# Performance work log

Measured on AMD Instinct MI355X. Metric: run time of the kernel, lower is better.

Reference implementation:

```python
import jax, jax.numpy as jnp
import numpy as np

VOCAB, EMBED, HIDDEN = 32000, 512, 1024
B, T = 2, 2048
LN_EPS = 1e-5


def setup_inputs() -> dict:
    key = jax.random.key(0)
    ks = jax.random.split(key, 12)

    def xavier(k, fan_in, fan_out):
        lim = float(np.sqrt(6.0 / (fan_in + fan_out)))
        return jax.random.uniform(k, (fan_in, fan_out), jnp.float32, -lim, lim)

    return {
        "tokens": jax.random.randint(ks[0], (B, T), 0, VOCAB),
        "E": xavier(ks[1], VOCAB, EMBED),                    # embedding table
        "Wc": xavier(ks[2], EMBED, HIDDEN),                  # fc_current (stored [in,out])
        "bc": jnp.full((HIDDEN,), 0.01, jnp.float32),
        "Wh": xavier(ks[3], EMBED, HIDDEN),                  # fc_context
        "bh": jnp.full((HIDDEN,), 0.01, jnp.float32),
        "Wm": xavier(ks[4], 2 * HIDDEN, HIDDEN),             # fc_merge
        "bm": jnp.full((HIDDEN,), 0.01, jnp.float32),
        "Wo": xavier(ks[5], HIDDEN, VOCAB),                  # fc_out
        "bo": jnp.full((VOCAB,), 0.01, jnp.float32),
        "ln_w": jnp.ones((HIDDEN,), jnp.float32),
        "ln_b": jnp.zeros((HIDDEN,), jnp.float32),
    }


def reference(tokens, E, Wc, bc, Wh, bh, Wm, bm, Wo, bo, ln_w, ln_b):
    emb = E[tokens]  # [B, T, D]
    # history mean at step t = mean(emb[:, :t]); at t==0 the module uses current embed
    csum = jnp.cumsum(emb, axis=1)
    counts = jnp.arange(1, T, dtype=emb.dtype)[None, :, None]
    hist_mean = jnp.concatenate([emb[:, :1], csum[:, :-1] / counts], axis=1)  # [B,T,D]

    cur_enc = jax.nn.relu(jnp.einsum("btd,dh->bth", emb, Wc) + bc)
    hist_enc = jax.nn.relu(jnp.einsum("btd,dh->bth", hist_mean, Wh) + bh)
    merged = jnp.concatenate([cur_enc, hist_enc], axis=-1)  # [B,T,2H]
    merged = jax.nn.relu(jnp.einsum("btk,kh->bth", merged, Wm) + bm)

    mu = jnp.mean(merged, axis=-1, keepdims=True)
    var = jnp.mean(jnp.square(merged - mu), axis=-1, keepdims=True)
    normed = (merged - mu) * jax.lax.rsqrt(var + LN_EPS) * ln_w + ln_b

    logits = (jnp.einsum("bth,hv->btv", normed, Wo) + bo) / 10.0  # [B,T,V]
    return logits
```

## Files before the change

### kernel.cpp

```cpp
#include <hip/hip_runtime.h>
#include <hip/hip_bf16.h>
#include <stdint.h>
#include <stdio.h>

#define T_SEQ  2048
#define BATCH  2
#define NROWS  4096
#define EMBED  512
#define HIDDEN 1024
#define VOCAB  32000
#define NCHUNK 32
#define CHLEN  64

typedef __bf16 bf16x8 __attribute__((ext_vector_type(8)));
typedef float  f32x4  __attribute__((ext_vector_type(4)));

__device__ __forceinline__ float b2f(unsigned short h) {
  union { unsigned int u; float f; } v; v.u = ((unsigned int)h) << 16; return v.f;
}
__device__ __forceinline__ unsigned short f2b(float f) {
  union { float f; unsigned int u; } v; v.f = f;
  unsigned int u = v.u;
  u += 0x7fffu + ((u >> 16) & 1u);
  return (unsigned short)(u >> 16);
}

__global__ void gather_kernel(const int* __restrict__ tokens,
                              const float* __restrict__ E,
                              unsigned short* __restrict__ emb) {
  const int row = blockIdx.x;
  const int tok = tokens[row];
  const float2 v = ((const float2*)(E + (size_t)tok * EMBED))[threadIdx.x];
  const uint32_t packed = (uint32_t)f2b(v.x) | ((uint32_t)f2b(v.y) << 16);
  ((uint32_t*)(emb + (size_t)row * EMBED))[threadIdx.x] = packed;
}

__global__ void scan_sum_kernel(const unsigned short* __restrict__ emb,
                                float* __restrict__ csum) {
  const int bc = blockIdx.x;
  const int d  = threadIdx.x;
  const unsigned short* e = emb + ((size_t)bc * CHLEN) * EMBED + d;
  float s = 0.f;
  #pragma unroll 8
  for (int i = 0; i < CHLEN; ++i) s += b2f(e[(size_t)i * EMBED]);
  csum[(size_t)bc * EMBED + d] = s;
}

__global__ void scan_excl_kernel(float* __restrict__ csum) {
  const int b = blockIdx.x;
  const int d = threadIdx.x;
  float run = 0.f;
  for (int c = 0; c < NCHUNK; ++c) {
    const size_t idx = ((size_t)b * NCHUNK + c) * EMBED + d;
    const float v = csum[idx];
    csum[idx] = run;
    run += v;
  }
}

__global__ void scan_emit_kernel(const unsigned short* __restrict__ emb,
                                 const float* __restrict__ csum,
                                 unsigned short* __restrict__ hist) {
  const int bc = blockIdx.x;
  const int c  = bc & (NCHUNK - 1);
  const int d  = threadIdx.x;
  const unsigned short* e = emb  + ((size_t)bc * CHLEN) * EMBED + d;
  unsigned short*       h = hist + ((size_t)bc * CHLEN) * EMBED + d;
  float sum = csum[(size_t)bc * EMBED + d];
  #pragma unroll 8
  for (int i = 0; i < CHLEN; ++i) {
    const int t = c * CHLEN + i;
    h[(size_t)i * EMBED] = (t == 0) ? e[0] : f2b(sum / (float)t);
    sum += b2f(e[(size_t)i * EMBED]);
  }
}

__global__ void transpose_cast_kernel(const float* __restrict__ in,
                                      unsigned short* __restrict__ out,
                                      int R, int C) {
  __shared__ float tile[32][33];
  const int tx = threadIdx.x & 31;
  const int ty = threadIdx.x >> 5;
  const int r0 = blockIdx.y * 32, c0 = blockIdx.x * 32;
  #pragma unroll
  for (int i = 0; i < 32; i += 8)
    tile[ty + i][tx] = in[(size_t)(r0 + ty + i) * C + (c0 + tx)];
  __syncthreads();
  #pragma unroll
  for (int i = 0; i < 32; i += 8)
    out[(size_t)(c0 + ty + i) * R + (r0 + tx)] = f2b(tile[tx][ty + i]);
}

#define BM 128
#define BN 128
#define BK 32

__device__ __forceinline__ void async16(unsigned short* lds, const unsigned short* g) {
  __builtin_amdgcn_global_load_lds(
      (const __attribute__((address_space(1))) void*)g,
      (__attribute__((address_space(3))) void*)lds, 16, 0, 0);
}

template<int MODE>
__global__ __launch_bounds__(256) void gemm_bt_kernel(
    const unsigned short* __restrict__ A,
    const unsigned short* __restrict__ BT,
    const float* __restrict__ bias,
    void* __restrict__ out, int M, int N, int K, int ldOut, int colOff) {
  __shared__ unsigned short As[BM * BK];
  __shared__ unsigned short Bs[BN * BK];

  const int tid  = threadIdx.x;
  const int wave = tid >> 6;
  const int lane = tid & 63;
  const int m0 = blockIdx.y * BM;
  const int n0 = blockIdx.x * BN;
  const int wm = (wave & 1) * 64;
  const int wn = (wave >> 1) * 64;

  const int srow = (wave << 5) + (lane >> 2);
  const int scol = (lane & 3) << 3;
  const unsigned short* aSrc = A  + (size_t)(m0 + srow) * K + scol;
  const unsigned short* bSrc = BT + (size_t)(n0 + srow) * K + scol;
  unsigned short* aDst = As + (wave << 5) * BK;
  unsigned short* bDst = Bs + (wave << 5) * BK;

  f32x4 acc[4][4];
  #pragma unroll
  for (int i = 0; i < 4; ++i)
    #pragma unroll
    for (int j = 0; j < 4; ++j)
      acc[i][j] = (f32x4){0.f, 0.f, 0.f, 0.f};

  const int q = lane >> 4;
  const int r = lane & 15;

  for (int k0 = 0; k0 < K; k0 += BK) {
    __syncthreads();
    async16(aDst,           aSrc);
    async16(aDst + 16 * BK, aSrc + 16 * (size_t)K);
    async16(bDst,           bSrc);
    async16(bDst + 16 * BK, bSrc + 16 * (size_t)K);
    aSrc += BK; bSrc += BK;
    __syncthreads();

    bf16x8 af[4], bfr[4];
    #pragma unroll
    for (int mi = 0; mi < 4; ++mi)
      af[mi] = *(const bf16x8*)&As[(wm + mi * 16 + r) * BK + (q << 3)];
    #pragma unroll
    for (int ni = 0; ni < 4; ++ni)
      bfr[ni] = *(const bf16x8*)&Bs[(wn + ni * 16 + r) * BK + (q << 3)];
    #pragma unroll
    for (int mi = 0; mi < 4; ++mi)
      #pragma unroll
      for (int ni = 0; ni < 4; ++ni)
        acc[mi][ni] = __builtin_amdgcn_mfma_f32_16x16x32_bf16(
            af[mi], bfr[ni], acc[mi][ni], 0, 0, 0);
  }

  #pragma unroll
  for (int ni = 0; ni < 4; ++ni) {
    const int col = n0 + wn + ni * 16 + r;
    const float bv = bias[col];
    #pragma unroll
    for (int mi = 0; mi < 4; ++mi) {
      #pragma unroll
      for (int e = 0; e < 4; ++e) {
        const int row = m0 + wm + mi * 16 + (q << 2) + e;
        float v = acc[mi][ni][e] + bv;
        if (MODE == 0 || MODE == 1) v = fmaxf(v, 0.f);
        if (MODE == 2) v *= 0.1f;
        const size_t idx = (size_t)row * ldOut + colOff + col;
        if (MODE == 0) ((unsigned short*)out)[idx] = f2b(v);
        else           ((float*)out)[idx] = v;
      }
    }
  }
}

__global__ void ln_kernel(const float* __restrict__ merged,
                          const float* __restrict__ lnw,
                          const float* __restrict__ lnb,
                          unsigned short* __restrict__ normed) {
  const int row = blockIdx.x;
  const float4 v = ((const float4*)(merged + (size_t)row * HIDDEN))[threadIdx.x];
  float s  = v.x + v.y + v.z + v.w;
  float ss = v.x * v.x + v.y * v.y + v.z * v.z + v.w * v.w;
  #pragma unroll
  for (int off = 32; off > 0; off >>= 1) {
    s  += __shfl_down(s, off, 64);
    ss += __shfl_down(ss, off, 64);
  }
  __shared__ float red[8];
  const int wvi = threadIdx.x >> 6;
  if ((threadIdx.x & 63) == 0) { red[wvi] = s; red[4 + wvi] = ss; }
  __syncthreads();
  s  = red[0] + red[1] + red[2] + red[3];
  ss = red[4] + red[5] + red[6] + red[7];
  const float mu  = s * (1.0f / HIDDEN);
  const float var = ss * (1.0f / HIDDEN) - mu * mu;
  const float rs  = rsqrtf(var + 1e-5f);
  const float4 w4 = ((const float4*)lnw)[threadIdx.x];
  const float4 b4 = ((const float4*)lnb)[threadIdx.x];
  ushort4 o;
  o.x = f2b((v.x - mu) * rs * w4.x + b4.x);
  o.y = f2b((v.y - mu) * rs * w4.y + b4.y);
  o.z = f2b((v.z - mu) * rs * w4.z + b4.z);
  o.w = f2b((v.w - mu) * rs * w4.w + b4.w);
  ((ushort4*)(normed + (size_t)row * HIDDEN))[threadIdx.x] = o;
}

extern "C" void kernel_launch(void* const* d_in, const int* in_sizes, int n_in,
                              void* d_out, int out_size, void* d_ws, size_t ws_size,
                              hipStream_t stream) {
  const int*   tokens = (const int*)d_in[0];
  const float* E      = (const float*)d_in[1];
  const float* Wc     = (const float*)d_in[2];
  const float* bc     = (const float*)d_in[3];
  const float* Wh     = (const float*)d_in[4];
  const float* bh     = (const float*)d_in[5];
  const float* Wm     = (const float*)d_in[6];
  const float* bm     = (const float*)d_in[7];
  const float* Wo     = (const float*)d_in[8];
  const float* bo     = (const float*)d_in[9];
  const float* lnw    = (const float*)d_in[10];
  const float* lnb    = (const float*)d_in[11];

  char* p = (char*)d_ws;
  unsigned short* WcT  = (unsigned short*)p; p += (size_t)HIDDEN * EMBED * 2;
  unsigned short* WhT  = (unsigned short*)p; p += (size_t)HIDDEN * EMBED * 2;
  unsigned short* WmT  = (unsigned short*)p; p += (size_t)HIDDEN * (2 * HIDDEN) * 2;
  unsigned short* WoT  = (unsigned short*)p; p += (size_t)VOCAB * HIDDEN * 2;
  unsigned short* emb  = (unsigned short*)p; p += (size_t)NROWS * EMBED * 2;
  unsigned short* hist = (unsigned short*)p; p += (size_t)NROWS * EMBED * 2;
  unsigned short* cat  = (unsigned short*)p; p += (size_t)NROWS * (2 * HIDDEN) * 2;
  float*          mrg  = (float*)p;          p += (size_t)NROWS * HIDDEN * 4;
  unsigned short* nrm  = (unsigned short*)p; p += (size_t)NROWS * HIDDEN * 2;
  float*          csum = (float*)p;          p += (size_t)BATCH * NCHUNK * EMBED * 4;
  if ((size_t)(p - (char*)d_ws) > ws_size)
    fprintf(stderr, "WS TOO SMALL: need %zu have %zu\n", (size_t)(p - (char*)d_ws), ws_size);

  transpose_cast_kernel<<<dim3(HIDDEN / 32, EMBED / 32), 256, 0, stream>>>(Wc, WcT, EMBED, HIDDEN);
  transpose_cast_kernel<<<dim3(HIDDEN / 32, EMBED / 32), 256, 0, stream>>>(Wh, WhT, EMBED, HIDDEN);
  transpose_cast_kernel<<<dim3(HIDDEN / 32, (2 * HIDDEN) / 32), 256, 0, stream>>>(Wm, WmT, 2 * HIDDEN, HIDDEN);
  transpose_cast_kernel<<<dim3(VOCAB / 32, HIDDEN / 32), 256, 0, stream>>>(Wo, WoT, HIDDEN, VOCAB);

  gather_kernel<<<NROWS, 256, 0, stream>>>(tokens, E, emb);
  scan_sum_kernel <<<BATCH * NCHUNK, EMBED, 0, stream>>>(emb, csum);
  scan_excl_kernel<<<BATCH, EMBED, 0, stream>>>(csum);
  scan_emit_kernel<<<BATCH * NCHUNK, EMBED, 0, stream>>>(emb, csum, hist);

  gemm_bt_kernel<0><<<dim3(HIDDEN / BN, NROWS / BM), 256, 0, stream>>>(
      emb, WcT, bc, cat, NROWS, HIDDEN, EMBED, 2 * HIDDEN, 0);
  gemm_bt_kernel<0><<<dim3(HIDDEN / BN, NROWS / BM), 256, 0, stream>>>(
      hist, WhT, bh, cat, NROWS, HIDDEN, EMBED, 2 * HIDDEN, HIDDEN);
  gemm_bt_kernel<1><<<dim3(HIDDEN / BN, NROWS / BM), 256, 0, stream>>>(
      cat, WmT, bm, mrg, NROWS, HIDDEN, 2 * HIDDEN, HIDDEN, 0);
  ln_kernel<<<NROWS, 256, 0, stream>>>(mrg, lnw, lnb, nrm);
  gemm_bt_kernel<2><<<dim3(VOCAB / BN, NROWS / BM), 256, 0, stream>>>(
      nrm, WoT, bo, d_out, NROWS, VOCAB, HIDDEN, VOCAB, 0);
}
```

Before: 1.135 ms.

## Remap GEMM workgroups per XCD, batch encoder GEMMs, use nontemporal logit stores

```diff
diff --git a/kernel.cpp b/kernel.cpp
--- a/kernel.cpp
+++ b/kernel.cpp
@@ -106,22 +106,42 @@
     const unsigned short* __restrict__ A,
     const unsigned short* __restrict__ BT,
     const float* __restrict__ bias,
-    void* __restrict__ out, int M, int N, int K, int ldOut, int colOff) {
+    void* __restrict__ out, int M, int N, int K, int ldOut, int colOff,
+    const unsigned short* __restrict__ A2,
+    const unsigned short* __restrict__ BT2,
+    const float* __restrict__ bias2, int colOff2) {
   __shared__ unsigned short As[BM * BK];
   __shared__ unsigned short Bs[BN * BK];
+
+  const unsigned short* Ap = A;
+  const unsigned short* Bp = BT;
+  const float*          bp = bias;
+  int                   co = colOff;
+  if (blockIdx.z) { Ap = A2; Bp = BT2; bp = bias2; co = colOff2; }
+
+  int wg = blockIdx.x;
+  {
+    const int nwg = gridDim.x;
+    const int xcd = wg & 7, loc = wg >> 3;
+    const int q = nwg >> 3, r = nwg & 7;
+    wg = (xcd < r ? xcd * (q + 1) : r * (q + 1) + (xcd - r) * q) + loc;
+  }
+  const int nmb = M / BM;
+  const int mb  = wg % nmb;
+  const int nb  = wg / nmb;
+  const int m0  = mb * BM;
+  const int n0  = nb * BN;
 
   const int tid  = threadIdx.x;
   const int wave = tid >> 6;
   const int lane = tid & 63;
-  const int m0 = blockIdx.y * BM;
-  const int n0 = blockIdx.x * BN;
   const int wm = (wave & 1) * 64;
   const int wn = (wave >> 1) * 64;
 
   const int srow = (wave << 5) + (lane >> 2);
   const int scol = (lane & 3) << 3;
-  const unsigned short* aSrc = A  + (size_t)(m0 + srow) * K + scol;
-  const unsigned short* bSrc = BT + (size_t)(n0 + srow) * K + scol;
+  const unsigned short* aSrc = Ap + (size_t)(m0 + srow) * K + scol;
+  const unsigned short* bSrc = Bp + (size_t)(n0 + srow) * K + scol;
   unsigned short* aDst = As + (wave << 5) * BK;
   unsigned short* bDst = Bs + (wave << 5) * BK;
 
@@ -162,7 +182,7 @@
   #pragma unroll
   for (int ni = 0; ni < 4; ++ni) {
     const int col = n0 + wn + ni * 16 + r;
-    const float bv = bias[col];
+    const float bv = bp[col];
     #pragma unroll
     for (int mi = 0; mi < 4; ++mi) {
       #pragma unroll
@@ -171,9 +191,10 @@
         float v = acc[mi][ni][e] + bv;
         if (MODE == 0 || MODE == 1) v = fmaxf(v, 0.f);
         if (MODE == 2) v *= 0.1f;
-        const size_t idx = (size_t)row * ldOut + colOff + col;
-        if (MODE == 0) ((unsigned short*)out)[idx] = f2b(v);
-        else           ((float*)out)[idx] = v;
+        const size_t idx = (size_t)row * ldOut + co + col;
+        if (MODE == 0)      ((unsigned short*)out)[idx] = f2b(v);
+        else if (MODE == 1) ((float*)out)[idx] = v;
+        else                __builtin_nontemporal_store(v, &((float*)out)[idx]);
       }
     }
   }
@@ -251,13 +272,17 @@
   scan_excl_kernel<<<BATCH, EMBED, 0, stream>>>(csum);
   scan_emit_kernel<<<BATCH * NCHUNK, EMBED, 0, stream>>>(emb, csum, hist);
 
-  gemm_bt_kernel<0><<<dim3(HIDDEN / BN, NROWS / BM), 256, 0, stream>>>(
-      emb, WcT, bc, cat, NROWS, HIDDEN, EMBED, 2 * HIDDEN, 0);
-  gemm_bt_kernel<0><<<dim3(HIDDEN / BN, NROWS / BM), 256, 0, stream>>>(
-      hist, WhT, bh, cat, NROWS, HIDDEN, EMBED, 2 * HIDDEN, HIDDEN);
-  gemm_bt_kernel<1><<<dim3(HIDDEN / BN, NROWS / BM), 256, 0, stream>>>(
-      cat, WmT, bm, mrg, NROWS, HIDDEN, 2 * HIDDEN, HIDDEN, 0);
+  const int nwgEnc = (NROWS / BM) * (HIDDEN / BN);
+  const int nwgOut = (NROWS / BM) * (VOCAB / BN);
+
+  gemm_bt_kernel<0><<<dim3(nwgEnc, 1, 2), 256, 0, stream>>>(
+      emb, WcT, bc, cat, NROWS, HIDDEN, EMBED, 2 * HIDDEN, 0,
+      hist, WhT, bh, HIDDEN);
+  gemm_bt_kernel<1><<<dim3(nwgEnc, 1, 1), 256, 0, stream>>>(
+      cat, WmT, bm, mrg, NROWS, HIDDEN, 2 * HIDDEN, HIDDEN, 0,
+      nullptr, nullptr, nullptr, 0);
   ln_kernel<<<NROWS, 256, 0, stream>>>(mrg, lnw, lnb, nrm);
-  gemm_bt_kernel<2><<<dim3(VOCAB / BN, NROWS / BM), 256, 0, stream>>>(
-      nrm, WoT, bo, d_out, NROWS, VOCAB, HIDDEN, VOCAB, 0);
-}
+  gemm_bt_kernel<2><<<dim3(nwgOut, 1, 1), 256, 0, stream>>>(
+      nrm, WoT, bo, d_out, NROWS, VOCAB, HIDDEN, VOCAB, 0,
+      nullptr, nullptr, nullptr, 0);
+}
```

After: 1.080 ms. 1.05x faster.
